# Kernel optimization log

Measured on AMD Instinct MI355X. Metric: run time of the kernel, lower is better.

## Reference

```python
import jax, jax.numpy as jnp
import numpy as np

N_CELLS = 100000
CHANNELS = 64
NNZ = 1600000


def _spmm(rows, cols, vals, x, n):
    # y[i] = sum_{k: rows[k]==i} vals[k] * x[cols[k]]  -- sparse Laplacian matvec over features
    return jax.ops.segment_sum(vals[:, None] * x[cols], rows, num_segments=n)


def setup_inputs() -> dict:
    key = jax.random.key(0)
    ks = jax.random.split(key, 9)
    scale = 1.0 / np.sqrt(CHANNELS)
    return {
        "x": jax.random.normal(ks[0], (N_CELLS, CHANNELS), dtype=jnp.float32),
        "down_rows": jax.random.randint(ks[1], (NNZ,), 0, N_CELLS, dtype=jnp.int32),
        "down_cols": jax.random.randint(ks[2], (NNZ,), 0, N_CELLS, dtype=jnp.int32),
        "down_vals": jax.random.normal(ks[3], (NNZ,), dtype=jnp.float32),
        "up_rows": jax.random.randint(ks[4], (NNZ,), 0, N_CELLS, dtype=jnp.int32),
        "up_cols": jax.random.randint(ks[5], (NNZ,), 0, N_CELLS, dtype=jnp.int32),
        "up_vals": jax.random.normal(ks[6], (NNZ,), dtype=jnp.float32),
        "w_conv": jax.random.normal(ks[7], (CHANNELS, CHANNELS), dtype=jnp.float32) * scale,
        "w_lin": jax.random.normal(ks[8], (CHANNELS, CHANNELS), dtype=jnp.float32) * scale,
    }


def reference(x, down_rows, down_cols, down_vals, up_rows, up_cols, up_vals, w_conv, w_lin):
    n = x.shape[0]
    xw = x @ w_conv  # shared Conv weight for both Laplacian paths
    x_down = _spmm(down_rows, down_cols, down_vals, xw, n)  # L_down @ (x W_conv)
    x_up = _spmm(up_rows, up_cols, up_vals, xw, n)          # L_up   @ (x W_conv)
    x_id = x @ w_lin                                         # bias-free Linear
    # Aggregation(update_func='sigmoid'): sum messages then activate
    return jax.nn.sigmoid(x_down + x_up + x_id)
```

## Files before the change

### kernel.cpp

```cpp
#include <hip/hip_runtime.h>
#include <hip/hip_bf16.h>
#include <hip/hip_fp16.h>

#define CH 64
#define RPB 128
#define RPB_SH 7
#define MAXNB 800
#define CAPG 4352
#define BATCH 4096
#define SPILLMAX 16384
#define FILL_BLOCKS 391
#define GEMM_PHYS 512
#define NVB (GEMM_PHYS * 2)

typedef __attribute__((ext_vector_type(8))) _Float16 half8;
typedef __attribute__((ext_vector_type(4))) float f32x4;

#define COLOFF_MASK 0x00FFFF80

__global__ __launch_bounds__(512) void gemm_fill_kernel(
    const float* __restrict__ x, const float* __restrict__ wc,
    const float* __restrict__ wl, __half* __restrict__ xwh,
    float* __restrict__ out, int n,
    const int* __restrict__ r1, const int* __restrict__ c1, const float* __restrict__ v1,
    const int* __restrict__ r2, const int* __restrict__ c2, const float* __restrict__ v2,
    int* __restrict__ gcur, int* __restrict__ spillcnt, int4* __restrict__ spill,
    int2* __restrict__ ebuf, int nnz, int nb) {
  __shared__ int2 stash[BATCH];
  __shared__ unsigned short sbuck[BATCH];
  __shared__ int hist[MAXNB];
  __shared__ int rbase[MAXNB];

  const int tid = threadIdx.x;

  if (blockIdx.x < (unsigned)FILL_BLOCKS) {
    const int tot = 2 * nnz;
    const int nbatches = (tot + BATCH - 1) / BATCH;
    for (int bt = blockIdx.x; bt < nbatches; bt += FILL_BLOCKS) {
      for (int i = tid; i < nb; i += 512) hist[i] = 0;
      __syncthreads();

      const int e0 = bt * BATCH;
      const int m = min(BATCH, tot - e0);
      for (int i = tid; i < m; i += 512) {
        const int e = e0 + i;
        int r, c;
        float v;
        if (e < nnz) {
          r = r1[e]; c = c1[e]; v = v1[e];
        } else {
          r = r2[e - nnz]; c = c2[e - nnz]; v = v2[e - nnz];
        }
        const int b = r >> RPB_SH;
        stash[i] = make_int2(((r & (RPB - 1)) << 24) | (c << 7), __float_as_int(v));
        sbuck[i] = (unsigned short)b;
        atomicAdd(&hist[b], 1);
      }
      __syncthreads();

      for (int b = tid; b < nb; b += 512) {
        const int c = hist[b];
        rbase[b] = c ? atomicAdd(&gcur[b], c) : 0;
        hist[b] = 0;
      }
      __syncthreads();

      for (int i = tid; i < m; i += 512) {
        const int b = sbuck[i];
        const int2 rec = stash[i];
        const int p = rbase[b] + atomicAdd(&hist[b], 1);
        if (p < CAPG) {
          ebuf[(size_t)b * CAPG + p] = rec;
        } else {
          const int sp = atomicAdd(spillcnt, 1);
          if (sp < SPILLMAX)
            spill[sp] = make_int4(b * RPB + (rec.x >> 24), rec.x & COLOFF_MASK,
                                  rec.y, 0);
        }
      }
      __syncthreads();
    }
    return;
  }

  const int vb = (int)(blockIdx.x - FILL_BLOCKS) * 2 + (tid >> 8);
  const int t256 = tid & 255;
  const int lane = t256 & 63;
  const int wv = t256 >> 6;
  const int mat = wv >> 1;
  const int tile = wv & 1;
  const float* __restrict__ W = mat ? wl : wc;

  const int i16 = lane & 15;
  const int kseg = lane >> 4;

  half8 bhi[4][2], blo[4][2];
#pragma unroll
  for (int nt = 0; nt < 4; ++nt)
#pragma unroll
    for (int kk = 0; kk < 2; ++kk)
#pragma unroll
      for (int j = 0; j < 8; ++j) {
        const float w = W[(kk * 32 + kseg * 8 + j) * CH + nt * 16 + i16];
        const _Float16 hh = (_Float16)w;
        bhi[nt][kk][j] = hh;
        blo[nt][kk][j] = (_Float16)(w - (float)hh);
      }

  const int ngroups = (n + 31) >> 5;
  for (int g = vb; g < ngroups; g += NVB) {
    const int base = g * 32 + tile * 16;
    const int row = base + i16;
    const int rowc = (row < n) ? row : (n - 1);
    const float* xp = x + (size_t)rowc * CH + kseg * 8;

    float af[16];
    {
      const float4 p0 = *(const float4*)(xp);
      const float4 p1 = *(const float4*)(xp + 4);
      const float4 q0 = *(const float4*)(xp + 32);
      const float4 q1 = *(const float4*)(xp + 36);
      af[0] = p0.x; af[1] = p0.y; af[2] = p0.z; af[3] = p0.w;
      af[4] = p1.x; af[5] = p1.y; af[6] = p1.z; af[7] = p1.w;
      af[8] = q0.x; af[9] = q0.y; af[10] = q0.z; af[11] = q0.w;
      af[12] = q1.x; af[13] = q1.y; af[14] = q1.z; af[15] = q1.w;
    }
    half8 ahi[2], alo[2];
#pragma unroll
    for (int kk = 0; kk < 2; ++kk)
#pragma unroll
      for (int j = 0; j < 8; ++j) {
        const float f = af[kk * 8 + j];
        const _Float16 hh = (_Float16)f;
        ahi[kk][j] = hh;
        alo[kk][j] = (_Float16)(f - (float)hh);
      }

    f32x4 acc[4];
#pragma unroll
    for (int nt = 0; nt < 4; ++nt) {
      f32x4 a = {0.f, 0.f, 0.f, 0.f};
#pragma unroll
      for (int kk = 0; kk < 2; ++kk) {
        a = __builtin_amdgcn_mfma_f32_16x16x32_f16(ahi[kk], bhi[nt][kk], a, 0, 0, 0);
        a = __builtin_amdgcn_mfma_f32_16x16x32_f16(alo[kk], bhi[nt][kk], a, 0, 0, 0);
        a = __builtin_amdgcn_mfma_f32_16x16x32_f16(ahi[kk], blo[nt][kk], a, 0, 0, 0);
      }
      acc[nt] = a;
    }

    if (mat == 0) {
#pragma unroll
      for (int nt = 0; nt < 4; ++nt)
#pragma unroll
        for (int r = 0; r < 4; ++r) {
          const int orow = base + kseg * 4 + r;
          if (orow < n)
            xwh[(size_t)orow * CH + nt * 16 + i16] = __float2half(acc[nt][r]);
        }
    } else {
#pragma unroll
      for (int nt = 0; nt < 4; ++nt)
#pragma unroll
        for (int r = 0; r < 4; ++r) {
          const int orow = base + kseg * 4 + r;
          if (orow < n)
            out[(size_t)orow * CH + nt * 16 + i16] = acc[nt][r];
        }
    }
  }
}

__global__ __launch_bounds__(512) void sortB_kernel(
    const int* __restrict__ gcur, int2* __restrict__ ebuf,
    unsigned int* __restrict__ rowinfo, int n, int nb) {
  __shared__ int2 raw[CAPG];
  __shared__ int hist[RPB];
  __shared__ int sc[RPB];
  __shared__ int cur[RPB];
  const int b = blockIdx.x;
  const int beg = b * CAPG;
  const int cnt = min(gcur[b], CAPG);

  if (threadIdx.x < RPB) hist[threadIdx.x] = 0;
  __syncthreads();

  for (int i = threadIdx.x; i < cnt; i += 512) {
    const int2 rec = ebuf[beg + i];
    raw[i] = rec;
    atomicAdd(&hist[rec.x >> 24], 1);
  }
  __syncthreads();

  int v = 0;
  if (threadIdx.x < RPB) {
    v = hist[threadIdx.x];
    sc[threadIdx.x] = v;
  }
  __syncthreads();
  for (int off = 1; off < RPB; off <<= 1) {
    int t = 0;
    if (threadIdx.x < RPB && threadIdx.x >= off) t = sc[threadIdx.x - off];
    __syncthreads();
    if (threadIdx.x < RPB) sc[threadIdx.x] += t;
    __syncthreads();
  }
  if (threadIdx.x < RPB) {
    const int ex = sc[threadIdx.x] - v;
    cur[threadIdx.x] = ex;
    const int gr = b * RPB + threadIdx.x;
    if (gr < n) rowinfo[gr] = ((unsigned int)ex << 16) | (unsigned int)v;
  }
  __syncthreads();

  for (int i = threadIdx.x; i < cnt; i += 512) {
    const int2 rec = raw[i];
    const int pos = atomicAdd(&cur[rec.x >> 24], 1);
    ebuf[beg + pos] = rec;
  }
}

union U8 {
  uint4 u4;
  __half h[8];
};

__device__ __forceinline__ void edge_fma(float* a, const U8& u, float v) {
#pragma unroll
  for (int k = 0; k < 8; ++k)
    a[k] = fmaf(v, __half2float(u.h[k]), a[k]);
}

__global__ __launch_bounds__(256) void gather_kernel(
    const unsigned int* __restrict__ rowinfo, const int2* __restrict__ ebuf,
    const char* __restrict__ xwbytes, float4* __restrict__ outf4,
    const int* __restrict__ spillcnt, const int4* __restrict__ spill,
    int n) {
  const int lane = threadIdx.x & 63;
  const int g = lane >> 3;
  const int l8 = lane & 7;
  const int l8b = l8 << 4;
  const int w = (blockIdx.x * blockDim.x + threadIdx.x) >> 6;
  const int nw = (gridDim.x * blockDim.x) >> 6;
  const int sc = min(*spillcnt, SPILLMAX);

  for (int row = w; row < n; row += nw) {
    const float4 lin0 = outf4[(size_t)row * 16 + 2 * l8];
    const float4 lin1 = outf4[(size_t)row * 16 + 2 * l8 + 1];

    float a[8];
#pragma unroll
    for (int k = 0; k < 8; ++k) a[k] = 0.f;

    const unsigned int info = rowinfo[row];
    const int beg = (row >> RPB_SH) * CAPG + (int)(info >> 16);
    const int end = beg + (int)(info & 0xFFFFu);

    int e = beg;
    for (; e + 16 <= end; e += 16) {
      const int2 rc0 = ebuf[e + g];
      const int2 rc1 = ebuf[e + 8 + g];
      U8 u0, u1;
      u0.u4 = *(const uint4*)(xwbytes + (rc0.x & COLOFF_MASK) + l8b);
      u1.u4 = *(const uint4*)(xwbytes + (rc1.x & COLOFF_MASK) + l8b);
      edge_fma(a, u0, __int_as_float(rc0.y));
      edge_fma(a, u1, __int_as_float(rc1.y));
    }
    for (; e < end; e += 8) {
      const int idx = e + g;
      const bool ok = idx < end;
      const int2 rc = ebuf[ok ? idx : (end - 1)];
      U8 u;
      u.u4 = *(const uint4*)(xwbytes + (rc.x & COLOFF_MASK) + l8b);
      edge_fma(a, u, ok ? __int_as_float(rc.y) : 0.f);
    }

    if (sc > 0) {
      for (int s = 0; s < sc; ++s) {
        const int4 r = spill[s];
        if (r.x == row && g == 0) {
          U8 u;
          u.u4 = *(const uint4*)(xwbytes + r.y + l8b);
          edge_fma(a, u, __int_as_float(r.z));
        }
      }
    }

#pragma unroll
    for (int k = 0; k < 8; ++k) {
      a[k] += __shfl_xor(a[k], 8, 64);
      a[k] += __shfl_xor(a[k], 16, 64);
      a[k] += __shfl_xor(a[k], 32, 64);
    }

    if (lane < 8) {
      float4 o0, o1;
      o0.x = 1.f / (1.f + __expf(-(lin0.x + a[0])));
      o0.y = 1.f / (1.f + __expf(-(lin0.y + a[1])));
      o0.z = 1.f / (1.f + __expf(-(lin0.z + a[2])));
      o0.w = 1.f / (1.f + __expf(-(lin0.w + a[3])));
      o1.x = 1.f / (1.f + __expf(-(lin1.x + a[4])));
      o1.y = 1.f / (1.f + __expf(-(lin1.y + a[5])));
      o1.z = 1.f / (1.f + __expf(-(lin1.z + a[6])));
      o1.w = 1.f / (1.f + __expf(-(lin1.w + a[7])));
      outf4[(size_t)row * 16 + 2 * l8] = o0;
      outf4[(size_t)row * 16 + 2 * l8 + 1] = o1;
    }
  }
}

__global__ __launch_bounds__(256) void gemm_kernel(
    const float* __restrict__ x, const float* __restrict__ wc,
    const float* __restrict__ wl, __half* __restrict__ xwh,
    float* __restrict__ out, int n) {
  const int lane = threadIdx.x & 63;
  const int wv = threadIdx.x >> 6;
  const int mat = wv >> 1;
  const int tile = wv & 1;
  const float* __restrict__ W = mat ? wl : wc;
  const int i16 = lane & 15;
  const int kseg = lane >> 4;

  half8 bhi[4][2], blo[4][2];
#pragma unroll
  for (int nt = 0; nt < 4; ++nt)
#pragma unroll
    for (int kk = 0; kk < 2; ++kk)
#pragma unroll
      for (int j = 0; j < 8; ++j) {
        const float w = W[(kk * 32 + kseg * 8 + j) * CH + nt * 16 + i16];
        const _Float16 hh = (_Float16)w;
        bhi[nt][kk][j] = hh;
        blo[nt][kk][j] = (_Float16)(w - (float)hh);
      }

  const int ngroups = (n + 31) >> 5;
  for (int g = blockIdx.x; g < ngroups; g += gridDim.x) {
    const int base = g * 32 + tile * 16;
    const int row = base + i16;
    const int rowc = (row < n) ? row : (n - 1);
    const float* xp = x + (size_t)rowc * CH + kseg * 8;
    float af[16];
    {
      const float4 p0 = *(const float4*)(xp);
      const float4 p1 = *(const float4*)(xp + 4);
      const float4 q0 = *(const float4*)(xp + 32);
      const float4 q1 = *(const float4*)(xp + 36);
      af[0] = p0.x; af[1] = p0.y; af[2] = p0.z; af[3] = p0.w;
      af[4] = p1.x; af[5] = p1.y; af[6] = p1.z; af[7] = p1.w;
      af[8] = q0.x; af[9] = q0.y; af[10] = q0.z; af[11] = q0.w;
      af[12] = q1.x; af[13] = q1.y; af[14] = q1.z; af[15] = q1.w;
    }
    half8 ahi[2], alo[2];
#pragma unroll
    for (int kk = 0; kk < 2; ++kk)
#pragma unroll
      for (int j = 0; j < 8; ++j) {
        const float f = af[kk * 8 + j];
        const _Float16 hh = (_Float16)f;
        ahi[kk][j] = hh;
        alo[kk][j] = (_Float16)(f - (float)hh);
      }
    f32x4 acc[4];
#pragma unroll
    for (int nt = 0; nt < 4; ++nt) {
      f32x4 a = {0.f, 0.f, 0.f, 0.f};
#pragma unroll
      for (int kk = 0; kk < 2; ++kk) {
        a = __builtin_amdgcn_mfma_f32_16x16x32_f16(ahi[kk], bhi[nt][kk], a, 0, 0, 0);
        a = __builtin_amdgcn_mfma_f32_16x16x32_f16(alo[kk], bhi[nt][kk], a, 0, 0, 0);
        a = __builtin_amdgcn_mfma_f32_16x16x32_f16(ahi[kk], blo[nt][kk], a, 0, 0, 0);
      }
      acc[nt] = a;
    }
    if (mat == 0) {
#pragma unroll
      for (int nt = 0; nt < 4; ++nt)
#pragma unroll
        for (int r = 0; r < 4; ++r) {
          const int orow = base + kseg * 4 + r;
          if (orow < n)
            xwh[(size_t)orow * CH + nt * 16 + i16] = __float2half(acc[nt][r]);
        }
    } else {
#pragma unroll
      for (int nt = 0; nt < 4; ++nt)
#pragma unroll
        for (int r = 0; r < 4; ++r) {
          const int orow = base + kseg * 4 + r;
          if (orow < n)
            out[(size_t)orow * CH + nt * 16 + i16] = acc[nt][r];
        }
    }
  }
}

__global__ __launch_bounds__(256) void scatter_kernel(
    const int* __restrict__ rows, const int* __restrict__ cols,
    const float* __restrict__ vals, const __half* __restrict__ xwh,
    float* __restrict__ out, int nnz) {
  const int lane = threadIdx.x & 63;
  const int wid = (blockIdx.x * blockDim.x + threadIdx.x) >> 6;
  const int nwaves = (gridDim.x * blockDim.x) >> 6;
  for (int k = wid; k < nnz; k += nwaves) {
    const float xv = __half2float(xwh[(size_t)cols[k] * CH + lane]);
    atomicAdd(&out[(size_t)rows[k] * CH + lane], vals[k] * xv);
  }
}

__global__ __launch_bounds__(256) void sigmoid_kernel(float* __restrict__ out, int n4) {
  const int i = blockIdx.x * blockDim.x + threadIdx.x;
  if (i < n4) {
    float4 v = reinterpret_cast<float4*>(out)[i];
    v.x = 1.f / (1.f + __expf(-v.x));
    v.y = 1.f / (1.f + __expf(-v.y));
    v.z = 1.f / (1.f + __expf(-v.z));
    v.w = 1.f / (1.f + __expf(-v.w));
    reinterpret_cast<float4*>(out)[i] = v;
  }
}

extern "C" void kernel_launch(void* const* d_in, const int* in_sizes, int n_in,
                              void* d_out, int out_size, void* d_ws, size_t ws_size,
                              hipStream_t stream) {
  const float* x         = (const float*)d_in[0];
  const int*   down_rows = (const int*)d_in[1];
  const int*   down_cols = (const int*)d_in[2];
  const float* down_vals = (const float*)d_in[3];
  const int*   up_rows   = (const int*)d_in[4];
  const int*   up_cols   = (const int*)d_in[5];
  const float* up_vals   = (const float*)d_in[6];
  const float* w_conv    = (const float*)d_in[7];
  const float* w_lin     = (const float*)d_in[8];

  const int n   = in_sizes[0] / CH;
  const int nnz = in_sizes[1];
  const int nb  = (n + RPB - 1) / RPB;

  float* out = (float*)d_out;

  char* p = (char*)d_ws;
  __half* xwh  = (__half*)p;  p += (size_t)n * CH * 2;
  int* gcur    = (int*)p;  p += (size_t)nb * 4;
  int* spillc  = (int*)p;  p += 16;
  unsigned int* rowinfo = (unsigned int*)p;  p += ((size_t)n + 2) * 4;
  p = (char*)(((uintptr_t)p + 15) & ~(uintptr_t)15);
  int4* spill  = (int4*)p; p += (size_t)SPILLMAX * 16;
  int2* ebuf   = (int2*)p; p += (size_t)nb * CAPG * 8;
  const size_t need = (size_t)(p - (char*)d_ws);

  if (ws_size >= need && nb <= MAXNB && n < (1 << 17)) {
    hipMemsetAsync(gcur, 0, (size_t)nb * 4 + 16, stream);
    gemm_fill_kernel<<<FILL_BLOCKS + GEMM_PHYS, 512, 0, stream>>>(
        x, w_conv, w_lin, xwh, out, n,
        down_rows, down_cols, down_vals, up_rows, up_cols, up_vals,
        gcur, spillc, spill, ebuf, nnz, nb);
    sortB_kernel<<<nb, 512, 0, stream>>>(gcur, ebuf, rowinfo, n, nb);
    const int nblk = (n + 3) / 4;
    gather_kernel<<<nblk, 256, 0, stream>>>(rowinfo, ebuf, (const char*)xwh,
                                            (float4*)out, spillc, spill, n);
  } else {
    gemm_kernel<<<1024, 256, 0, stream>>>(x, w_conv, w_lin, xwh, out, n);
    scatter_kernel<<<4096, 256, 0, stream>>>(down_rows, down_cols, down_vals, xwh, out, nnz);
    scatter_kernel<<<4096, 256, 0, stream>>>(up_rows, up_cols, up_vals, xwh, out, nnz);
    const int n4 = (n * CH) / 4;
    sigmoid_kernel<<<(n4 + 255) / 256, 256, 0, stream>>>(out, n4);
  }
}
```

Before: 141.2 us.

## Process four rows per wave in gather and drop LDS staging in bucket sort

The gather kernel now has each wavefront handle four consecutive rows in lockstep, issuing four independent edge and feature loads per iteration. This raises memory-level parallelism and hides gather latency. The bucket sort no longer stages records in a 35 KB shared array. It re-reads them from global memory and writes the sorted copy into a separate ebuf2 buffer, trading extra global traffic and workspace for higher occupancy. Rows of unequal length waste lanes, because every row in a group iterates to the longest row's count.

```diff
diff --git a/kernel.cpp b/kernel.cpp
--- a/kernel.cpp
+++ b/kernel.cpp
@@ -171,10 +171,10 @@
   }
 }
 
-__global__ __launch_bounds__(512) void sortB_kernel(
-    const int* __restrict__ gcur, int2* __restrict__ ebuf,
-    unsigned int* __restrict__ rowinfo, int n, int nb) {
-  __shared__ int2 raw[CAPG];
+__global__ __launch_bounds__(512) void sortB2_kernel(
+    const int* __restrict__ gcur, const int2* __restrict__ ebuf,
+    int2* __restrict__ ebuf2, unsigned int* __restrict__ rowinfo,
+    int n, int nb) {
   __shared__ int hist[RPB];
   __shared__ int sc[RPB];
   __shared__ int cur[RPB];
@@ -185,11 +185,8 @@
   if (threadIdx.x < RPB) hist[threadIdx.x] = 0;
   __syncthreads();
 
-  for (int i = threadIdx.x; i < cnt; i += 512) {
-    const int2 rec = ebuf[beg + i];
-    raw[i] = rec;
-    atomicAdd(&hist[rec.x >> 24], 1);
-  }
+  for (int i = threadIdx.x; i < cnt; i += 512)
+    atomicAdd(&hist[ebuf[beg + i].x >> 24], 1);
   __syncthreads();
 
   int v = 0;
@@ -214,9 +211,9 @@
   __syncthreads();
 
   for (int i = threadIdx.x; i < cnt; i += 512) {
-    const int2 rec = raw[i];
+    const int2 rec = ebuf[beg + i];
     const int pos = atomicAdd(&cur[rec.x >> 24], 1);
-    ebuf[beg + pos] = rec;
+    ebuf2[beg + pos] = rec;
   }
 }
 
@@ -225,14 +222,8 @@
   __half h[8];
 };
 
-__device__ __forceinline__ void edge_fma(float* a, const U8& u, float v) {
-#pragma unroll
-  for (int k = 0; k < 8; ++k)
-    a[k] = fmaf(v, __half2float(u.h[k]), a[k]);
-}
-
 __global__ __launch_bounds__(256) void gather_kernel(
-    const unsigned int* __restrict__ rowinfo, const int2* __restrict__ ebuf,
+    const unsigned int* __restrict__ rowinfo, const int2* __restrict__ ebuf2,
     const char* __restrict__ xwbytes, float4* __restrict__ outf4,
     const int* __restrict__ spillcnt, const int4* __restrict__ spill,
     int n) {
@@ -242,69 +233,116 @@
   const int l8b = l8 << 4;
   const int w = (blockIdx.x * blockDim.x + threadIdx.x) >> 6;
   const int nw = (gridDim.x * blockDim.x) >> 6;
-  const int sc = min(*spillcnt, SPILLMAX);
-
-  for (int row = w; row < n; row += nw) {
-    const float4 lin0 = outf4[(size_t)row * 16 + 2 * l8];
-    const float4 lin1 = outf4[(size_t)row * 16 + 2 * l8 + 1];
-
-    float a[8];
-#pragma unroll
-    for (int k = 0; k < 8; ++k) a[k] = 0.f;
-
-    const unsigned int info = rowinfo[row];
-    const int beg = (row >> RPB_SH) * CAPG + (int)(info >> 16);
-    const int end = beg + (int)(info & 0xFFFFu);
-
-    int e = beg;
-    for (; e + 16 <= end; e += 16) {
-      const int2 rc0 = ebuf[e + g];
-      const int2 rc1 = ebuf[e + 8 + g];
-      U8 u0, u1;
-      u0.u4 = *(const uint4*)(xwbytes + (rc0.x & COLOFF_MASK) + l8b);
-      u1.u4 = *(const uint4*)(xwbytes + (rc1.x & COLOFF_MASK) + l8b);
-      edge_fma(a, u0, __int_as_float(rc0.y));
-      edge_fma(a, u1, __int_as_float(rc1.y));
-    }
-    for (; e < end; e += 8) {
-      const int idx = e + g;
-      const bool ok = idx < end;
-      const int2 rc = ebuf[ok ? idx : (end - 1)];
-      U8 u;
-      u.u4 = *(const uint4*)(xwbytes + (rc.x & COLOFF_MASK) + l8b);
-      edge_fma(a, u, ok ? __int_as_float(rc.y) : 0.f);
-    }
-
-    if (sc > 0) {
-      for (int s = 0; s < sc; ++s) {
+  const int scnt = min(*spillcnt, SPILLMAX);
+
+  for (int row0 = w * 4; row0 < n; row0 += nw * 4) {
+    float a0[8], a1[8], a2[8], a3[8];
+#pragma unroll
+    for (int k = 0; k < 8; ++k) { a0[k] = 0.f; a1[k] = 0.f; a2[k] = 0.f; a3[k] = 0.f; }
+
+    int e[4], end[4];
+    int iters = 0;
+#pragma unroll
+    for (int r = 0; r < 4; ++r) {
+      const int row = row0 + r;
+      if (row < n) {
+        const unsigned int info = rowinfo[row];
+        const int beg = (row >> RPB_SH) * CAPG + (int)(info >> 16);
+        const int c = (int)(info & 0xFFFFu);
+        e[r] = beg;
+        end[r] = beg + c;
+        const int it = (c + 7) >> 3;
+        iters = it > iters ? it : iters;
+      } else {
+        e[r] = 0; end[r] = 0;
+      }
+    }
+
+    for (int it = 0; it < iters; ++it) {
+      int2 rc[4];
+      U8 u[4];
+#pragma unroll
+      for (int r = 0; r < 4; ++r) {
+        const int idx = e[r] + g;
+        const int cidx = (idx < end[r]) ? idx : max(end[r] - 1, 0);
+        rc[r] = ebuf2[cidx];
+      }
+#pragma unroll
+      for (int r = 0; r < 4; ++r)
+        u[r].u4 = *(const uint4*)(xwbytes + (rc[r].x & COLOFF_MASK) + l8b);
+      {
+        const float v0 = (e[0] + g < end[0]) ? __int_as_float(rc[0].y) : 0.f;
+        const float v1 = (e[1] + g < end[1]) ? __int_as_float(rc[1].y) : 0.f;
+        const float v2 = (e[2] + g < end[2]) ? __int_as_float(rc[2].y) : 0.f;
+        const float v3 = (e[3] + g < end[3]) ? __int_as_float(rc[3].y) : 0.f;
+#pragma unroll
+        for (int k = 0; k < 8; ++k) {
+          a0[k] = fmaf(v0, __half2float(u[0].h[k]), a0[k]);
+          a1[k] = fmaf(v1, __half2float(u[1].h[k]), a1[k]);
+          a2[k] = fmaf(v2, __half2float(u[2].h[k]), a2[k]);
+          a3[k] = fmaf(v3, __half2float(u[3].h[k]), a3[k]);
+        }
+      }
+#pragma unroll
+      for (int r = 0; r < 4; ++r) e[r] += 8;
+    }
+
+    if (scnt > 0) {
+      for (int s = 0; s < scnt; ++s) {
         const int4 r = spill[s];
-        if (r.x == row && g == 0) {
+        if (g == 0 && r.x >= row0 && r.x < row0 + 4) {
           U8 u;
           u.u4 = *(const uint4*)(xwbytes + r.y + l8b);
-          edge_fma(a, u, __int_as_float(r.z));
+          const float v = __int_as_float(r.z);
+          const int ri = r.x - row0;
+#pragma unroll
+          for (int k = 0; k < 8; ++k) {
+            if (ri == 0) a0[k] = fmaf(v, __half2float(u.h[k]), a0[k]);
+            if (ri == 1) a1[k] = fmaf(v, __half2float(u.h[k]), a1[k]);
+            if (ri == 2) a2[k] = fmaf(v, __half2float(u.h[k]), a2[k]);
+            if (ri == 3) a3[k] = fmaf(v, __half2float(u.h[k]), a3[k]);
+          }
         }
       }
     }
 
 #pragma unroll
     for (int k = 0; k < 8; ++k) {
-      a[k] += __shfl_xor(a[k], 8, 64);
-      a[k] += __shfl_xor(a[k], 16, 64);
-      a[k] += __shfl_xor(a[k], 32, 64);
+      a0[k] += __shfl_xor(a0[k], 8, 64);
+      a0[k] += __shfl_xor(a0[k], 16, 64);
+      a0[k] += __shfl_xor(a0[k], 32, 64);
+      a1[k] += __shfl_xor(a1[k], 8, 64);
+      a1[k] += __shfl_xor(a1[k], 16, 64);
+      a1[k] += __shfl_xor(a1[k], 32, 64);
+      a2[k] += __shfl_xor(a2[k], 8, 64);
+      a2[k] += __shfl_xor(a2[k], 16, 64);
+      a2[k] += __shfl_xor(a2[k], 32, 64);
+      a3[k] += __shfl_xor(a3[k], 8, 64);
+      a3[k] += __shfl_xor(a3[k], 16, 64);
+      a3[k] += __shfl_xor(a3[k], 32, 64);
     }
 
     if (lane < 8) {
-      float4 o0, o1;
-      o0.x = 1.f / (1.f + __expf(-(lin0.x + a[0])));
-      o0.y = 1.f / (1.f + __expf(-(lin0.y + a[1])));
-      o0.z = 1.f / (1.f + __expf(-(lin0.z + a[2])));
-      o0.w = 1.f / (1.f + __expf(-(lin0.w + a[3])));
-      o1.x = 1.f / (1.f + __expf(-(lin1.x + a[4])));
-      o1.y = 1.f / (1.f + __expf(-(lin1.y + a[5])));
-      o1.z = 1.f / (1.f + __expf(-(lin1.z + a[6])));
-      o1.w = 1.f / (1.f + __expf(-(lin1.w + a[7])));
-      outf4[(size_t)row * 16 + 2 * l8] = o0;
-      outf4[(size_t)row * 16 + 2 * l8 + 1] = o1;
+#pragma unroll
+      for (int r = 0; r < 4; ++r) {
+        const int row = row0 + r;
+        if (row < n) {
+          const float* ar = (r == 0) ? a0 : (r == 1) ? a1 : (r == 2) ? a2 : a3;
+          const float4 lin0 = outf4[(size_t)row * 16 + 2 * l8];
+          const float4 lin1 = outf4[(size_t)row * 16 + 2 * l8 + 1];
+          float4 o0, o1;
+          o0.x = 1.f / (1.f + __expf(-(lin0.x + ar[0])));
+          o0.y = 1.f / (1.f + __expf(-(lin0.y + ar[1])));
+          o0.z = 1.f / (1.f + __expf(-(lin0.z + ar[2])));
+          o0.w = 1.f / (1.f + __expf(-(lin0.w + ar[3])));
+          o1.x = 1.f / (1.f + __expf(-(lin1.x + ar[4])));
+          o1.y = 1.f / (1.f + __expf(-(lin1.y + ar[5])));
+          o1.z = 1.f / (1.f + __expf(-(lin1.z + ar[6])));
+          o1.w = 1.f / (1.f + __expf(-(lin1.w + ar[7])));
+          outf4[(size_t)row * 16 + 2 * l8] = o0;
+          outf4[(size_t)row * 16 + 2 * l8 + 1] = o1;
+        }
+      }
     }
   }
 }
@@ -447,6 +485,7 @@
   p = (char*)(((uintptr_t)p + 15) & ~(uintptr_t)15);
   int4* spill  = (int4*)p; p += (size_t)SPILLMAX * 16;
   int2* ebuf   = (int2*)p; p += (size_t)nb * CAPG * 8;
+  int2* ebuf2  = (int2*)p; p += (size_t)nb * CAPG * 8;
   const size_t need = (size_t)(p - (char*)d_ws);
 
   if (ws_size >= need && nb <= MAXNB && n < (1 << 17)) {
@@ -455,9 +494,10 @@
         x, w_conv, w_lin, xwh, out, n,
         down_rows, down_cols, down_vals, up_rows, up_cols, up_vals,
         gcur, spillc, spill, ebuf, nnz, nb);
-    sortB_kernel<<<nb, 512, 0, stream>>>(gcur, ebuf, rowinfo, n, nb);
-    const int nblk = (n + 3) / 4;
-    gather_kernel<<<nblk, 256, 0, stream>>>(rowinfo, ebuf, (const char*)xwh,
+    sortB2_kernel<<<nb, 512, 0, stream>>>(gcur, ebuf, ebuf2, rowinfo, n, nb);
+    const int nwaves_needed = (n + 3) / 4;
+    const int nblk = (nwaves_needed + 3) / 4;
+    gather_kernel<<<nblk, 256, 0, stream>>>(rowinfo, ebuf2, (const char*)xwh,
                                             (float4*)out, spillc, spill, n);
   } else {
     gemm_kernel<<<1024, 256, 0, stream>>>(x, w_conv, w_lin, xwh, out, n);
```

Result: slower. 160.9 us (+13.9%).

## Sort edges out-of-place without LDS staging, rebalance fill/GEMM blocks

Applied to the files above, without the earlier changes.

The bucket sort now reads edges straight from global memory twice and writes the sorted records to a second buffer, so it no longer stages 4352 records in LDS. That frees shared memory, which should raise occupancy of the sort kernel. The gather kernel reads edge records as 64-bit nontemporal loads. The fill batch size and the fill/GEMM block split are also retuned. In exchange the sort does extra global reads and the workspace needs a second edge buffer.

```diff
diff --git a/kernel.cpp b/kernel.cpp
--- a/kernel.cpp
+++ b/kernel.cpp
@@ -7,10 +7,10 @@
 #define RPB_SH 7
 #define MAXNB 800
 #define CAPG 4352
-#define BATCH 4096
+#define BATCH 3072
 #define SPILLMAX 16384
-#define FILL_BLOCKS 391
-#define GEMM_PHYS 512
+#define FILL_BLOCKS 521
+#define GEMM_PHYS 503
 #define NVB (GEMM_PHYS * 2)
 
 typedef __attribute__((ext_vector_type(8))) _Float16 half8;
@@ -171,10 +171,10 @@
   }
 }
 
-__global__ __launch_bounds__(512) void sortB_kernel(
-    const int* __restrict__ gcur, int2* __restrict__ ebuf,
-    unsigned int* __restrict__ rowinfo, int n, int nb) {
-  __shared__ int2 raw[CAPG];
+__global__ __launch_bounds__(512) void sortB2_kernel(
+    const int* __restrict__ gcur, const int2* __restrict__ ebuf,
+    int2* __restrict__ ebuf2, unsigned int* __restrict__ rowinfo,
+    int n, int nb) {
   __shared__ int hist[RPB];
   __shared__ int sc[RPB];
   __shared__ int cur[RPB];
@@ -185,11 +185,8 @@
   if (threadIdx.x < RPB) hist[threadIdx.x] = 0;
   __syncthreads();
 
-  for (int i = threadIdx.x; i < cnt; i += 512) {
-    const int2 rec = ebuf[beg + i];
-    raw[i] = rec;
-    atomicAdd(&hist[rec.x >> 24], 1);
-  }
+  for (int i = threadIdx.x; i < cnt; i += 512)
+    atomicAdd(&hist[ebuf[beg + i].x >> 24], 1);
   __syncthreads();
 
   int v = 0;
@@ -214,9 +211,9 @@
   __syncthreads();
 
   for (int i = threadIdx.x; i < cnt; i += 512) {
-    const int2 rec = raw[i];
+    const int2 rec = ebuf[beg + i];
     const int pos = atomicAdd(&cur[rec.x >> 24], 1);
-    ebuf[beg + pos] = rec;
+    ebuf2[beg + pos] = rec;
   }
 }
 
@@ -232,7 +229,7 @@
 }
 
 __global__ __launch_bounds__(256) void gather_kernel(
-    const unsigned int* __restrict__ rowinfo, const int2* __restrict__ ebuf,
+    const unsigned int* __restrict__ rowinfo, const int2* __restrict__ ebuf2,
     const char* __restrict__ xwbytes, float4* __restrict__ outf4,
     const int* __restrict__ spillcnt, const int4* __restrict__ spill,
     int n) {
@@ -243,6 +240,8 @@
   const int w = (blockIdx.x * blockDim.x + threadIdx.x) >> 6;
   const int nw = (gridDim.x * blockDim.x) >> 6;
   const int sc = min(*spillcnt, SPILLMAX);
+  const unsigned long long* __restrict__ erec =
+      (const unsigned long long*)ebuf2;
 
   for (int row = w; row < n; row += nw) {
     const float4 lin0 = outf4[(size_t)row * 16 + 2 * l8];
@@ -258,21 +257,21 @@
 
     int e = beg;
     for (; e + 16 <= end; e += 16) {
-      const int2 rc0 = ebuf[e + g];
-      const int2 rc1 = ebuf[e + 8 + g];
+      const unsigned long long q0 = __builtin_nontemporal_load(&erec[e + g]);
+      const unsigned long long q1 = __builtin_nontemporal_load(&erec[e + 8 + g]);
       U8 u0, u1;
-      u0.u4 = *(const uint4*)(xwbytes + (rc0.x & COLOFF_MASK) + l8b);
-      u1.u4 = *(const uint4*)(xwbytes + (rc1.x & COLOFF_MASK) + l8b);
-      edge_fma(a, u0, __int_as_float(rc0.y));
-      edge_fma(a, u1, __int_as_float(rc1.y));
+      u0.u4 = *(const uint4*)(xwbytes + ((unsigned int)q0 & COLOFF_MASK) + l8b);
+      u1.u4 = *(const uint4*)(xwbytes + ((unsigned int)q1 & COLOFF_MASK) + l8b);
+      edge_fma(a, u0, __uint_as_float((unsigned int)(q0 >> 32)));
+      edge_fma(a, u1, __uint_as_float((unsigned int)(q1 >> 32)));
     }
     for (; e < end; e += 8) {
       const int idx = e + g;
       const bool ok = idx < end;
-      const int2 rc = ebuf[ok ? idx : (end - 1)];
+      const unsigned long long q = erec[ok ? idx : (end - 1)];
       U8 u;
-      u.u4 = *(const uint4*)(xwbytes + (rc.x & COLOFF_MASK) + l8b);
-      edge_fma(a, u, ok ? __int_as_float(rc.y) : 0.f);
+      u.u4 = *(const uint4*)(xwbytes + ((unsigned int)q & COLOFF_MASK) + l8b);
+      edge_fma(a, u, ok ? __uint_as_float((unsigned int)(q >> 32)) : 0.f);
     }
 
     if (sc > 0) {
@@ -447,17 +446,18 @@
   p = (char*)(((uintptr_t)p + 15) & ~(uintptr_t)15);
   int4* spill  = (int4*)p; p += (size_t)SPILLMAX * 16;
   int2* ebuf   = (int2*)p; p += (size_t)nb * CAPG * 8;
+  int2* ebuf2  = (int2*)p; p += (size_t)nb * CAPG * 8;
   const size_t need = (size_t)(p - (char*)d_ws);
 
   if (ws_size >= need && nb <= MAXNB && n < (1 << 17)) {
-    hipMemsetAsync(gcur, 0, (size_t)nb * 4 + 16, stream);
+    (void)hipMemsetAsync(gcur, 0, (size_t)nb * 4 + 16, stream);
     gemm_fill_kernel<<<FILL_BLOCKS + GEMM_PHYS, 512, 0, stream>>>(
         x, w_conv, w_lin, xwh, out, n,
         down_rows, down_cols, down_vals, up_rows, up_cols, up_vals,
         gcur, spillc, spill, ebuf, nnz, nb);
-    sortB_kernel<<<nb, 512, 0, stream>>>(gcur, ebuf, rowinfo, n, nb);
+    sortB2_kernel<<<nb, 512, 0, stream>>>(gcur, ebuf, ebuf2, rowinfo, n, nb);
     const int nblk = (n + 3) / 4;
-    gather_kernel<<<nblk, 256, 0, stream>>>(rowinfo, ebuf, (const char*)xwh,
+    gather_kernel<<<nblk, 256, 0, stream>>>(rowinfo, ebuf2, (const char*)xwh,
                                             (float4*)out, spillc, spill, n);
   } else {
     gemm_kernel<<<1024, 256, 0, stream>>>(x, w_conv, w_lin, xwh, out, n);
```

Result: slower. 153.2 us (+8.5%).
